# Optimization experiments

Measured on AMD Instinct MI355X. Metric: run time of the kernel, lower is better.

The kernel has to match this reference:

```python
import jax, jax.numpy as jnp
from jax import lax
import numpy as np

EPS = 1e-5

def _conv(x, w, b, s, p):
    # torch Conv2d: weight [O,I,kH,kW], NCHW
    y = lax.conv_general_dilated(x, w, (s, s), [(p, p), (p, p)],
                                 dimension_numbers=('NCHW', 'OIHW', 'NCHW'))
    return y + b[None, :, None, None]

def _convT(x, w, b, s, p):
    # torch ConvTranspose2d: weight [I,O,kH,kW]; equivalent to lhs-dilated conv
    wf = jnp.flip(w, (2, 3)).transpose(1, 0, 2, 3)  # -> [O,I,kH,kW]
    q = w.shape[2] - 1 - p
    y = lax.conv_general_dilated(x, wf, (1, 1), [(q, q), (q, q)],
                                 lhs_dilation=(s, s),
                                 dimension_numbers=('NCHW', 'OIHW', 'NCHW'))
    return y + b[None, :, None, None]

def _bn(x, g, b, m, v):
    # eval-mode BatchNorm2d with running stats
    s = g / jnp.sqrt(v + EPS)
    return x * s[None, :, None, None] + (b - m * s)[None, :, None, None]

def _forward(x, ew1, eb1, bn1g, bn1b, bn1m, bn1v, ew2, eb2, bn2g, bn2b, bn2m, bn2v,
             ew3, eb3, bn3g, bn3b, bn3m, bn3v, ew4, eb4, bn4g, bn4b, bn4m, bn4v,
             fc21w, fc21b, fc22w, fc22b, fc3w, fc3b,
             cw1, cb1, cbn1g, cbn1b, cbn1m, cbn1v, cw2, cb2, emb,
             dw1, db1, dbn1g, dbn1b, dbn1m, dbn1v, dw2, db2, dbn2g, dbn2b, dbn2m, dbn2v,
             dw3, db3, dbn3g, dbn3b, dbn3m, dbn3v, dw4, db4, dbn4g, dbn4b, dbn4m, dbn4v,
             ow, ob):
    relu = jax.nn.relu
    N = x.shape[0]
    # ---- encoder ----
    h = relu(_bn(_conv(x, ew1, eb1, 2, 1), bn1g, bn1b, bn1m, bn1v))   # [N,16,32,32]
    h = relu(_bn(_conv(h, ew2, eb2, 2, 1), bn2g, bn2b, bn2m, bn2v))   # [N,16,16,16]
    h = relu(_bn(_conv(h, ew3, eb3, 2, 1), bn3g, bn3b, bn3m, bn3v))   # [N,16,9,9]
    h = relu(_bn(_conv(h, ew4, eb4, 1, 0), bn4g, bn4b, bn4m, bn4v))   # [N,128,9,9]
    hl = h.reshape(N, -1)                                              # [N,10368]
    mu = hl @ fc21w + fc21b
    logvar = hl @ fc22w + fc22b
    z = mu  # eval-mode reparameterize returns mu
    # ---- vq_decode ----
    co = relu(z @ fc3w + fc3b)                                         # [N,10368]
    col = co.reshape(N, 128, 9, 9)
    ze = relu(_bn(_convT(col, cw1, cb1, 1, 0), cbn1g, cbn1b, cbn1m, cbn1v))
    z_e_x = _convT(ze, cw2, cb2, 1, 0)                                 # [N,32,9,9]
    zt = z_e_x.transpose(0, 2, 3, 1)                                   # [N,H,W,C]
    # ||z - e||^2 expanded (avoids [N,H,W,C,K] intermediate)
    d = ((zt * zt).sum(-1, keepdims=True)
         - 2.0 * jnp.einsum('nhwc,kc->nhwk', zt, emb)
         + (emb * emb).sum(-1))                                        # [N,H,W,K]
    latents = jnp.argmin(d, axis=-1)                                   # [N,H,W] int
    z_q = emb[latents]                                                 # [N,H,W,C]
    z_q_x = z_q.transpose(0, 3, 1, 2)                                  # [N,32,9,9]
    # ---- decoder ----
    g = relu(_bn(_convT(z_q_x, dw1, db1, 1, 0), dbn1g, dbn1b, dbn1m, dbn1v))  # [N,16,9,9]
    g = relu(_bn(_convT(g, dw2, db2, 2, 1), dbn2g, dbn2b, dbn2m, dbn2v))      # [N,16,18,18]
    g = relu(_bn(_convT(g, dw3, db3, 2, 1), dbn3g, dbn3b, dbn3m, dbn3v))      # [N,16,34,34]
    g = relu(_bn(_convT(g, dw4, db4, 2, 0), dbn4g, dbn4b, dbn4m, dbn4v))      # [N,16,68,68]
    x_tilde = _convT(g, ow, ob, 1, 0)                                         # [N,1,68,68]
    return (x_tilde, z, mu, logvar, z_e_x, z_q_x, latents)


def setup_inputs() -> dict:
    key = jax.random.key(0)
    ks = iter(jax.random.split(key, 64))
    def rn(shape, scale=0.05):
        return scale * jax.random.normal(next(ks), shape, jnp.float32)
    inp = {'x': jax.random.normal(next(ks), (512, 1, 64, 64), jnp.float32)}
    wspecs = {
        'ew1': (16, 1, 4, 4), 'eb1': (16,), 'ew2': (16, 16, 4, 4), 'eb2': (16,),
        'ew3': (16, 16, 2, 2), 'eb3': (16,), 'ew4': (128, 16, 1, 1), 'eb4': (128,),
        'fc21w': (10368, 64), 'fc21b': (64,), 'fc22w': (10368, 64), 'fc22b': (64,),
        'fc3w': (64, 10368), 'fc3b': (10368,),
        'cw1': (128, 32, 1, 1), 'cb1': (32,), 'cw2': (32, 32, 1, 1), 'cb2': (32,),
        'dw1': (32, 16, 1, 1), 'db1': (16,), 'dw2': (16, 16, 4, 4), 'db2': (16,),
        'dw3': (16, 16, 2, 2), 'db3': (16,), 'dw4': (16, 16, 2, 2), 'db4': (16,),
        'ow': (16, 1, 1, 1),
    }
    for n, s in wspecs.items():
        inp[n] = rn(s)
    inp['ob'] = jnp.full((1,), 0.5, jnp.float32)
    for ch, pre in [(16, 'bn1'), (16, 'bn2'), (16, 'bn3'), (128, 'bn4'), (32, 'cbn1'),
                    (16, 'dbn1'), (16, 'dbn2'), (16, 'dbn3'), (16, 'dbn4')]:
        inp[pre + 'g'] = jnp.ones((ch,), jnp.float32)
        inp[pre + 'b'] = jnp.zeros((ch,), jnp.float32)
        inp[pre + 'm'] = jnp.zeros((ch,), jnp.float32)
        inp[pre + 'v'] = jnp.ones((ch,), jnp.float32)
    inp['emb'] = rn((512, 32), 1.0 / 512)
    return inp


def reference(x, ew1, eb1, bn1g, bn1b, bn1m, bn1v, ew2, eb2, bn2g, bn2b, bn2m, bn2v,
              ew3, eb3, bn3g, bn3b, bn3m, bn3v, ew4, eb4, bn4g, bn4b, bn4m, bn4v,
              fc21w, fc21b, fc22w, fc22b, fc3w, fc3b,
              cw1, cb1, cbn1g, cbn1b, cbn1m, cbn1v, cw2, cb2, emb,
              dw1, db1, dbn1g, dbn1b, dbn1m, dbn1v, dw2, db2, dbn2g, dbn2b, dbn2m, dbn2v,
              dw3, db3, dbn3g, dbn3b, dbn3m, dbn3v, dw4, db4, dbn4g, dbn4b, dbn4m, dbn4v,
              ow, ob):
    return _forward(x, ew1, eb1, bn1g, bn1b, bn1m, bn1v, ew2, eb2, bn2g, bn2b, bn2m, bn2v,
                    ew3, eb3, bn3g, bn3b, bn3m, bn3v, ew4, eb4, bn4g, bn4b, bn4m, bn4v,
                    fc21w, fc21b, fc22w, fc22b, fc3w, fc3b,
                    cw1, cb1, cbn1g, cbn1b, cbn1m, cbn1v, cw2, cb2, emb,
                    dw1, db1, dbn1g, dbn1b, dbn1m, dbn1v, dw2, db2, dbn2g, dbn2b, dbn2m, dbn2v,
                    dw3, db3, dbn3g, dbn3b, dbn3m, dbn3v, dw4, db4, dbn4g, dbn4b, dbn4m, dbn4v,
                    ow, ob)
```

## Files before the change

kernel.cpp:

```cpp
#include <hip/hip_runtime.h>
#include <math.h>
#include <float.h>

#define BN_EPS 1e-5f

__device__ __forceinline__ float bn_apply(float y, float g, float b, float m, float v) {
  float s = g / sqrtf(v + BN_EPS);
  return y * s + (b - m * s);
}

__global__ void k_conv1(const float* __restrict__ x, const float* __restrict__ w,
                        const float* __restrict__ bias,
                        const float* __restrict__ g, const float* __restrict__ bb,
                        const float* __restrict__ bm, const float* __restrict__ bv,
                        float* __restrict__ out) {
  int t = blockIdx.x * 256 + threadIdx.x;
  int xo = t & 31, yo = (t >> 5) & 31, n = t >> 10;
  int iy0 = 2 * yo - 1, ix0 = 2 * xo - 1;
  const float* xb = x + n * 4096;
  float p[16];
#pragma unroll
  for (int ky = 0; ky < 4; ++ky)
#pragma unroll
    for (int kx = 0; kx < 4; ++kx) {
      int iy = iy0 + ky, ix = ix0 + kx;
      bool ok = (iy >= 0) & (iy < 64) & (ix >= 0) & (ix < 64);
      p[ky * 4 + kx] = ok ? xb[iy * 64 + ix] : 0.0f;
    }
  float* ob = out + n * 16384 + yo * 32 + xo;
#pragma unroll
  for (int o = 0; o < 16; ++o) {
    float acc = bias[o];
#pragma unroll
    for (int k = 0; k < 16; ++k) acc += p[k] * w[o * 16 + k];
    acc = bn_apply(acc, g[o], bb[o], bm[o], bv[o]);
    ob[o * 1024] = fmaxf(acc, 0.0f);
  }
}

__global__ void __launch_bounds__(256) k_conv2(const float* __restrict__ A,
                        const float* __restrict__ w, const float* __restrict__ bias,
                        const float* __restrict__ g, const float* __restrict__ bb,
                        const float* __restrict__ bm, const float* __restrict__ bv,
                        float* __restrict__ out) {
  int t = threadIdx.x;
  int lane = t & 63;
  int og = __builtin_amdgcn_readfirstlane(t >> 6);
  int idx = blockIdx.x * 64 + lane;
  int n = idx >> 8, p = idx & 255;
  int yo = p >> 4, xo = p & 15;
  int iy0 = 2 * yo - 1, ix0 = 2 * xo - 1;
  const float* Ab = A + n * 16384;
  float acc[4];
#pragma unroll
  for (int oo = 0; oo < 4; ++oo) acc[oo] = bias[og * 4 + oo];
  for (int i = 0; i < 16; ++i) {
    const float* ch = Ab + i * 1024;
    float pv[16];
#pragma unroll
    for (int ky = 0; ky < 4; ++ky)
#pragma unroll
      for (int kx = 0; kx < 4; ++kx) {
        int iy = iy0 + ky, ix = ix0 + kx;
        bool ok = (iy >= 0) & (iy < 32) & (ix >= 0) & (ix < 32);
        pv[ky * 4 + kx] = ok ? ch[iy * 32 + ix] : 0.0f;
      }
    const float* wb = w + ((og * 4) * 16 + i) * 16;
#pragma unroll
    for (int oo = 0; oo < 4; ++oo) {
      const float* wo = wb + oo * 256;
#pragma unroll
      for (int k = 0; k < 16; ++k) acc[oo] = fmaf(pv[k], wo[k], acc[oo]);
    }
  }
  float* ob = out + n * 4096 + p;
#pragma unroll
  for (int oo = 0; oo < 4; ++oo) {
    int o = og * 4 + oo;
    float s = g[o] / sqrtf(bv[o] + BN_EPS);
    float sh = bb[o] - bm[o] * s;
    ob[o * 256] = fmaxf(acc[oo] * s + sh, 0.0f);
  }
}

__global__ void __launch_bounds__(256) k_c34(const float* __restrict__ in,
    const float* __restrict__ w3, const float* __restrict__ b3,
    const float* __restrict__ g3, const float* __restrict__ bb3,
    const float* __restrict__ bm3, const float* __restrict__ bv3,
    const float* __restrict__ w4, const float* __restrict__ b4,
    const float* __restrict__ g4, const float* __restrict__ bb4,
    const float* __restrict__ bm4, const float* __restrict__ bv4,
    float* __restrict__ hl) {
  __shared__ float xin[4096];
  __shared__ float w3s[1024];
  __shared__ float c3s[16 * 81];
  __shared__ float k3a[16], k3b[16];
  __shared__ float k4a[128], k4b[128];
  int bx = blockIdx.x;
  int n = bx >> 1, half = bx & 1;
  int t = threadIdx.x;
  {
    const float4* iv = (const float4*)(in + n * 4096);
    float4* xv = (float4*)xin;
#pragma unroll
    for (int q = 0; q < 4; ++q) xv[t + 256 * q] = iv[t + 256 * q];
    for (int i = t; i < 1024; i += 256) w3s[i] = w3[i];
  }
  if (t < 16) {
    float s = g3[t] / sqrtf(bv3[t] + BN_EPS);
    k3a[t] = s;
    k3b[t] = b3[t] * s + (bb3[t] - bm3[t] * s);
  } else if (t >= 64 && t < 192) {
    int o = t - 64;
    float s = g4[o] / sqrtf(bv4[o] + BN_EPS);
    k4a[o] = s;
    k4b[o] = b4[o] * s + (bb4[o] - bm4[o] * s);
  }
  __syncthreads();
  for (int idx = t; idx < 1296; idx += 256) {
    int o = idx / 81, p = idx - o * 81;
    int yo = p / 9, xo = p - yo * 9;
    int iy0 = 2 * yo - 1, ix0 = 2 * xo - 1;
    bool ytop = iy0 >= 0, ybot = iy0 + 1 < 16;
    bool xlft = ix0 >= 0, xrgt = ix0 + 1 < 16;
    int iyt = ytop ? iy0 : 0, iyb = ybot ? iy0 + 1 : 15;
    int ixl = xlft ? ix0 : 0, ixr = xrgt ? ix0 + 1 : 15;
    float acc = 0.0f;
#pragma unroll
    for (int i = 0; i < 16; ++i) {
      const float* ch = xin + i * 256;
      float p0 = (ytop & xlft) ? ch[iyt * 16 + ixl] : 0.0f;
      float p1 = (ytop & xrgt) ? ch[iyt * 16 + ixr] : 0.0f;
      float p2 = (ybot & xlft) ? ch[iyb * 16 + ixl] : 0.0f;
      float p3 = (ybot & xrgt) ? ch[iyb * 16 + ixr] : 0.0f;
      float4 wv = *(const float4*)&w3s[(o * 16 + i) * 4];
      acc += p0 * wv.x + p1 * wv.y + p2 * wv.z + p3 * wv.w;
    }
    c3s[idx] = fmaxf(acc * k3a[o] + k3b[o], 0.0f);
  }
  __syncthreads();
  int lane = t & 63;
  int og = __builtin_amdgcn_readfirstlane(t >> 6);
  int o0 = half * 64 + og * 16;
  float* ob = hl + n * 10368;
#pragma unroll
  for (int pass = 0; pass < 2; ++pass) {
    int p = pass * 64 + lane;
    bool ok = p < 81; int pc = ok ? p : 80;
    float acc[16];
#pragma unroll
    for (int oo = 0; oo < 16; ++oo) acc[oo] = 0.0f;
#pragma unroll
    for (int i = 0; i < 16; ++i) {
      float v = c3s[i * 81 + pc];
#pragma unroll
      for (int oo = 0; oo < 16; ++oo)
        acc[oo] = fmaf(v, w4[(o0 + oo) * 16 + i], acc[oo]);
    }
    if (ok) {
#pragma unroll
      for (int oo = 0; oo < 16; ++oo) {
        int o = o0 + oo;
        ob[o * 81 + p] = fmaxf(acc[oo] * k4a[o] + k4b[o], 0.0f);
      }
    }
  }
}

__global__ void __launch_bounds__(256) k_gemm1(const float* __restrict__ hl,
                                               const float* __restrict__ w21,
                                               const float* __restrict__ w22,
                                               float* __restrict__ part) {
  __shared__ __align__(16) float hs[27 * 68];
  __shared__ __align__(16) float wsh[27 * 128];
  int kc = blockIdx.x, nt = blockIdx.y, t = threadIdx.x;
  int n0 = nt * 64, k0 = kc * 162;
  int jg = t & 31, ng = t >> 5;
  float acc[8][4];
#pragma unroll
  for (int i = 0; i < 8; ++i)
#pragma unroll
    for (int q = 0; q < 4; ++q) acc[i][q] = 0.0f;
  float ph[7], pw[14];
  {
    int ks = k0;
#pragma unroll
    for (int q = 0; q < 7; ++q) {
      int idx = t + q * 256;
      if (idx < 1728) { int nr = idx / 27, kk = idx - nr * 27;
        ph[q] = hl[(n0 + nr) * 10368 + ks + kk]; }
    }
#pragma unroll
    for (int q = 0; q < 14; ++q) {
      int idx = t + q * 256;
      if (idx < 3456) { int r = idx >> 7, c = idx & 127;
        pw[q] = (c < 64) ? w21[(ks + r) * 64 + c] : w22[(ks + r) * 64 + (c - 64)]; }
    }
  }
  for (int s = 0; s < 6; ++s) {
    __syncthreads();
#pragma unroll
    for (int q = 0; q < 7; ++q) {
      int idx = t + q * 256;
      if (idx < 1728) { int nr = idx / 27, kk = idx - nr * 27; hs[kk * 68 + nr] = ph[q]; }
    }
#pragma unroll
    for (int q = 0; q < 14; ++q) {
      int idx = t + q * 256;
      if (idx < 3456) wsh[idx] = pw[q];
    }
    __syncthreads();
    if (s < 5) {
      int ks = k0 + (s + 1) * 27;
#pragma unroll
      for (int q = 0; q < 7; ++q) {
        int idx = t + q * 256;
        if (idx < 1728) { int nr = idx / 27, kk = idx - nr * 27;
          ph[q] = hl[(n0 + nr) * 10368 + ks + kk]; }
      }
#pragma unroll
      for (int q = 0; q < 14; ++q) {
        int idx = t + q * 256;
        if (idx < 3456) { int r = idx >> 7, c = idx & 127;
          pw[q] = (c < 64) ? w21[(ks + r) * 64 + c] : w22[(ks + r) * 64 + (c - 64)]; }
      }
    }
#pragma unroll 9
    for (int kk = 0; kk < 27; ++kk) {
      float4 h0 = *(const float4*)&hs[kk * 68 + ng * 8];
      float4 h1 = *(const float4*)&hs[kk * 68 + ng * 8 + 4];
      float4 wv = *(const float4*)&wsh[kk * 128 + jg * 4];
      float hv[8] = {h0.x, h0.y, h0.z, h0.w, h1.x, h1.y, h1.z, h1.w};
#pragma unroll
      for (int i = 0; i < 8; ++i) {
        acc[i][0] = fmaf(hv[i], wv.x, acc[i][0]);
        acc[i][1] = fmaf(hv[i], wv.y, acc[i][1]);
        acc[i][2] = fmaf(hv[i], wv.z, acc[i][2]);
        acc[i][3] = fmaf(hv[i], wv.w, acc[i][3]);
      }
    }
  }
#pragma unroll
  for (int i = 0; i < 8; ++i) {
    int n = n0 + ng * 8 + i;
    *(float4*)&part[(size_t)(kc * 512 + n) * 128 + jg * 4] =
        make_float4(acc[i][0], acc[i][1], acc[i][2], acc[i][3]);
  }
}

__global__ void k_fc_red(const float* __restrict__ part, const float* __restrict__ b21,
                         const float* __restrict__ b22, float* __restrict__ z,
                         float* __restrict__ mu, float* __restrict__ lv) {
  int t = blockIdx.x * 256 + threadIdx.x;
  int j = t & 127, n = t >> 7;
  float s = 0.0f;
  for (int kc = 0; kc < 64; ++kc) s += part[(size_t)(kc * 512 + n) * 128 + j];
  if (j < 64) { float r = s + b21[j]; z[n * 64 + j] = r; mu[n * 64 + j] = r; }
  else        { lv[n * 64 + (j - 64)] = s + b22[j - 64]; }
}

__global__ void k_fc3(const float* __restrict__ z, const float* __restrict__ w,
                      const float* __restrict__ b, float* __restrict__ E) {
  int m = blockIdx.x * 128 + threadIdx.x;
  int n0 = blockIdx.y * 32;
  float acc[32];
#pragma unroll
  for (int nn = 0; nn < 32; ++nn) acc[nn] = 0.0f;
  for (int j = 0; j < 64; ++j) {
    float wv = w[j * 10368 + m];
    const float* zb = z + n0 * 64 + j;
#pragma unroll
    for (int nn = 0; nn < 32; ++nn) acc[nn] += zb[nn * 64] * wv;
  }
  float bvv = b[m];
  float* Eb = E + n0 * 10368 + m;
#pragma unroll
  for (int nn = 0; nn < 32; ++nn) Eb[nn * 10368] = fmaxf(acc[nn] + bvv, 0.0f);
}

__global__ void __launch_bounds__(256) k_cw(const float* __restrict__ E,
                     const float* __restrict__ w1, const float* __restrict__ b1,
                     const float* __restrict__ g, const float* __restrict__ bb,
                     const float* __restrict__ bm, const float* __restrict__ bv,
                     const float* __restrict__ w2, const float* __restrict__ b2,
                     float* __restrict__ zex, float* __restrict__ zt) {
  __shared__ float ze_s[2592];
  int n = blockIdx.x, t = threadIdx.x;
  int lane = t & 63;
  int o0 = __builtin_amdgcn_readfirstlane(t >> 6) * 8;
  const float* co = E + n * 10368;
#pragma unroll
  for (int pass = 0; pass < 2; ++pass) {
    int p = pass * 64 + lane;
    bool ok = p < 81; int pc = ok ? p : 80;
    float acc[8];
#pragma unroll
    for (int oo = 0; oo < 8; ++oo) acc[oo] = b1[o0 + oo];
    for (int i = 0; i < 128; ++i) {
      float v = co[i * 81 + pc];
#pragma unroll
      for (int oo = 0; oo < 8; ++oo)
        acc[oo] = fmaf(v, w1[i * 32 + o0 + oo], acc[oo]);
    }
#pragma unroll
    for (int oo = 0; oo < 8; ++oo) {
      int o = o0 + oo;
      float r = bn_apply(acc[oo], g[o], bb[o], bm[o], bv[o]);
      if (ok) ze_s[o * 81 + p] = fmaxf(r, 0.0f);
    }
  }
  __syncthreads();
  float* zb = zex + n * 2592;
  float* ztb = zt + n * 81 * 32;
#pragma unroll
  for (int pass = 0; pass < 2; ++pass) {
    int p = pass * 64 + lane;
    bool ok = p < 81; int pc = ok ? p : 80;
    float acc[8];
#pragma unroll
    for (int oo = 0; oo < 8; ++oo) acc[oo] = b2[o0 + oo];
    for (int j = 0; j < 32; ++j) {
      float v = ze_s[j * 81 + pc];
#pragma unroll
      for (int oo = 0; oo < 8; ++oo)
        acc[oo] = fmaf(v, w2[j * 32 + o0 + oo], acc[oo]);
    }
    if (ok) {
#pragma unroll
      for (int oo = 0; oo < 8; ++oo) {
        zb[(o0 + oo) * 81 + p] = acc[oo];
        ztb[p * 32 + o0 + oo] = acc[oo];
      }
    }
  }
}

__global__ void k_ee(const float* __restrict__ emb, float* __restrict__ ee) {
  int k = blockIdx.x * 256 + threadIdx.x;
  if (k < 512) {
    const float4* e = (const float4*)(emb + k * 32);
    float s = 0.0f;
#pragma unroll
    for (int q = 0; q < 8; ++q) {
      float4 v = e[q];
      s += v.x * v.x + v.y * v.y + v.z * v.z + v.w * v.w;
    }
    ee[k] = s;
  }
}

__global__ void __launch_bounds__(256) k_vq2(const float* __restrict__ zt,
                                             const float* __restrict__ emb,
                                             const float* __restrict__ ee,
                                             float* __restrict__ lat_out,
                                             float* __restrict__ zqx) {
  __shared__ float bd_s[4][64];
  __shared__ int   bi_s[4][64];
  __shared__ int   bif[64];
  int t = threadIdx.x;
  int lane = t & 63, sub = t >> 6;
  int sub_u = __builtin_amdgcn_readfirstlane(sub);
  int pix = blockIdx.x * 64 + lane;
  float z[32];
  {
    const float4* zr = (const float4*)(zt + (size_t)pix * 32);
#pragma unroll
    for (int q = 0; q < 8; ++q) {
      float4 v = zr[q];
      z[q * 4] = v.x; z[q * 4 + 1] = v.y; z[q * 4 + 2] = v.z; z[q * 4 + 3] = v.w;
    }
  }
  const float* ebase = emb + sub_u * 128 * 32;
  const float* eeb   = ee + sub_u * 128;
  int kbase = sub_u * 128;
  float best = FLT_MAX;
  int bi = kbase;
  for (int kk = 0; kk < 128; kk += 2) {
    const float* e0 = ebase + kk * 32;
    const float* e1 = e0 + 32;
    float d0a = 0.f, d0b = 0.f, d1a = 0.f, d1b = 0.f;
#pragma unroll
    for (int c = 0; c < 32; c += 2) {
      d0a = fmaf(z[c], e0[c], d0a);
      d0b = fmaf(z[c + 1], e0[c + 1], d0b);
      d1a = fmaf(z[c], e1[c], d1a);
      d1b = fmaf(z[c + 1], e1[c + 1], d1b);
    }
    float d0 = fmaf(-2.0f, d0a + d0b, eeb[kk]);
    float d1 = fmaf(-2.0f, d1a + d1b, eeb[kk + 1]);
    if (d0 < best) { best = d0; bi = kbase + kk; }
    if (d1 < best) { best = d1; bi = kbase + kk + 1; }
  }
  bd_s[sub][lane] = best;
  bi_s[sub][lane] = bi;
  __syncthreads();
  if (t < 64) {
    float bd = bd_s[0][t]; int b = bi_s[0][t];
#pragma unroll
    for (int q = 1; q < 4; ++q)
      if (bd_s[q][t] < bd) { bd = bd_s[q][t]; b = bi_s[q][t]; }
    lat_out[blockIdx.x * 64 + t] = (float)b;
    bif[t] = b;
  }
  __syncthreads();
  int pix0 = blockIdx.x * 64;
  for (int idx = t; idx < 2048; idx += 256) {
    int c = idx >> 6, pl = idx & 63;
    int pg = pix0 + pl;
    int n = pg / 81, p = pg - n * 81;
    zqx[n * 2592 + c * 81 + p] = emb[bif[pl] * 32 + c];
  }
}

__global__ void k_dw1(const float* __restrict__ in, const float* __restrict__ w,
                      const float* __restrict__ bias,
                      const float* __restrict__ g, const float* __restrict__ bb,
                      const float* __restrict__ bm, const float* __restrict__ bv,
                      float* __restrict__ out) {
  __shared__ float ws[512];
  for (int i = threadIdx.x; i < 512; i += 256) ws[i] = w[i];
  __syncthreads();
  int t = blockIdx.x * 256 + threadIdx.x;
  int p = t % 81; int o = (t / 81) & 15; int n = t / 1296;
  const float* ib = in + n * 2592 + p;
  float acc = bias[o];
#pragma unroll
  for (int i = 0; i < 32; ++i) acc += ib[i * 81] * ws[i * 16 + o];
  float r = bn_apply(acc, g[o], bb[o], bm[o], bv[o]);
  out[t] = fmaxf(r, 0.0f);
}

__global__ void __launch_bounds__(256) k_dw2(const float* __restrict__ in,
                      const float* __restrict__ w, const float* __restrict__ bias,
                      const float* __restrict__ g, const float* __restrict__ bb,
                      const float* __restrict__ bm, const float* __restrict__ bv,
                      float* __restrict__ out) {
  int t = threadIdx.x;
  int lane = t & 63;
  int og = __builtin_amdgcn_readfirstlane(t >> 6);
  int idx = blockIdx.x * 64 + lane;
  int n = idx / 81, blk = idx - n * 81;
  int iy = blk / 9, ix = blk - iy * 9;
  const float* ib = in + n * 1296;
  int r0 = iy - 1, r2 = iy + 1, c0 = ix - 1, c2 = ix + 1;
  bool r0ok = r0 >= 0, r2ok = r2 < 9, c0ok = c0 >= 0, c2ok = c2 < 9;
  int r0c = r0ok ? r0 : 0, r2c = r2ok ? r2 : 8;
  int c0c = c0ok ? c0 : 0, c2c = c2ok ? c2 : 8;
  float acc[4][2][2];
#pragma unroll
  for (int oo = 0; oo < 4; ++oo)
#pragma unroll
    for (int dy = 0; dy < 2; ++dy)
#pragma unroll
      for (int dx = 0; dx < 2; ++dx) acc[oo][dy][dx] = 0.0f;
  for (int i = 0; i < 16; ++i) {
    const float* ch = ib + i * 81;
    float v[3][3];
    v[1][1] = ch[iy * 9 + ix];
    v[1][0] = c0ok ? ch[iy * 9 + c0c] : 0.0f;
    v[1][2] = c2ok ? ch[iy * 9 + c2c] : 0.0f;
    v[0][1] = r0ok ? ch[r0c * 9 + ix] : 0.0f;
    v[0][0] = (r0ok & c0ok) ? ch[r0c * 9 + c0c] : 0.0f;
    v[0][2] = (r0ok & c2ok) ? ch[r0c * 9 + c2c] : 0.0f;
    v[2][1] = r2ok ? ch[r2c * 9 + ix] : 0.0f;
    v[2][0] = (r2ok & c0ok) ? ch[r2c * 9 + c0c] : 0.0f;
    v[2][2] = (r2ok & c2ok) ? ch[r2c * 9 + c2c] : 0.0f;
    const float* wb = w + (i * 16 + og * 4) * 16;
#pragma unroll
    for (int oo = 0; oo < 4; ++oo) {
      const float* wo = wb + oo * 16;
      acc[oo][0][0] = fmaf(v[1][1], wo[1 * 4 + 1], acc[oo][0][0]);
      acc[oo][0][0] = fmaf(v[1][0], wo[1 * 4 + 3], acc[oo][0][0]);
      acc[oo][0][0] = fmaf(v[0][1], wo[3 * 4 + 1], acc[oo][0][0]);
      acc[oo][0][0] = fmaf(v[0][0], wo[3 * 4 + 3], acc[oo][0][0]);
      acc[oo][0][1] = fmaf(v[1][1], wo[1 * 4 + 2], acc[oo][0][1]);
      acc[oo][0][1] = fmaf(v[1][2], wo[1 * 4 + 0], acc[oo][0][1]);
      acc[oo][0][1] = fmaf(v[0][1], wo[3 * 4 + 2], acc[oo][0][1]);
      acc[oo][0][1] = fmaf(v[0][2], wo[3 * 4 + 0], acc[oo][0][1]);
      acc[oo][1][0] = fmaf(v[1][1], wo[2 * 4 + 1], acc[oo][1][0]);
      acc[oo][1][0] = fmaf(v[1][0], wo[2 * 4 + 3], acc[oo][1][0]);
      acc[oo][1][0] = fmaf(v[2][1], wo[0 * 4 + 1], acc[oo][1][0]);
      acc[oo][1][0] = fmaf(v[2][0], wo[0 * 4 + 3], acc[oo][1][0]);
      acc[oo][1][1] = fmaf(v[1][1], wo[2 * 4 + 2], acc[oo][1][1]);
      acc[oo][1][1] = fmaf(v[1][2], wo[2 * 4 + 0], acc[oo][1][1]);
      acc[oo][1][1] = fmaf(v[2][1], wo[0 * 4 + 2], acc[oo][1][1]);
      acc[oo][1][1] = fmaf(v[2][2], wo[0 * 4 + 0], acc[oo][1][1]);
    }
  }
  float* ob = out + n * 5184 + (2 * iy) * 18 + 2 * ix;
#pragma unroll
  for (int oo = 0; oo < 4; ++oo) {
    int o = og * 4 + oo;
    float s = g[o] / sqrtf(bv[o] + BN_EPS);
    float sh = bb[o] - bm[o] * s;
    float bo = bias[o];
    float r00 = fmaxf((acc[oo][0][0] + bo) * s + sh, 0.0f);
    float r01 = fmaxf((acc[oo][0][1] + bo) * s + sh, 0.0f);
    float r10 = fmaxf((acc[oo][1][0] + bo) * s + sh, 0.0f);
    float r11 = fmaxf((acc[oo][1][1] + bo) * s + sh, 0.0f);
    float* op = ob + o * 324;
    *(float2*)&op[0]  = make_float2(r00, r01);
    *(float2*)&op[18] = make_float2(r10, r11);
  }
}

__global__ void k_dw3(const float* __restrict__ in, const float* __restrict__ w,
                      const float* __restrict__ bias,
                      const float* __restrict__ g, const float* __restrict__ bb,
                      const float* __restrict__ bm, const float* __restrict__ bv,
                      float* __restrict__ out) {
  int t = blockIdx.x * 256 + threadIdx.x;
  int ii = t % 324; int n = t / 324;
  int iy = ii / 18, ix = ii % 18;
  const float* ib = in + n * 5184 + iy * 18 + ix;
  float acc[4][16];
#pragma unroll
  for (int a = 0; a < 4; ++a)
#pragma unroll
    for (int o = 0; o < 16; ++o) acc[a][o] = 0.0f;
  for (int i = 0; i < 16; ++i) {
    float v = ib[i * 324];
    const float4* wr = (const float4*)(w + i * 64);
#pragma unroll
    for (int o = 0; o < 16; ++o) {
      float4 wt = wr[o];
      acc[0][o] = fmaf(v, wt.x, acc[0][o]);
      acc[1][o] = fmaf(v, wt.y, acc[1][o]);
      acc[2][o] = fmaf(v, wt.z, acc[2][o]);
      acc[3][o] = fmaf(v, wt.w, acc[3][o]);
    }
  }
  int yo0 = 2 * iy - 1, xo0 = 2 * ix - 1;
  float* ob = out + n * 18496;
#pragma unroll
  for (int o = 0; o < 16; ++o) {
    float s = g[o] / sqrtf(bv[o] + BN_EPS);
    float sh = bb[o] - bm[o] * s;
    float bo = bias[o];
#pragma unroll
    for (int a = 0; a < 2; ++a)
#pragma unroll
      for (int b = 0; b < 2; ++b) {
        int yo = yo0 + a, xo = xo0 + b;
        if (yo >= 0 && yo < 34 && xo >= 0 && xo < 34)
          ob[o * 1156 + yo * 34 + xo] = fmaxf((acc[a * 2 + b][o] + bo) * s + sh, 0.0f);
      }
  }
}

__global__ void k_dw4ow(const float* __restrict__ in, const float* __restrict__ w,
                        const float* __restrict__ bias,
                        const float* __restrict__ g, const float* __restrict__ bb,
                        const float* __restrict__ bm, const float* __restrict__ bv,
                        const float* __restrict__ oww, const float* __restrict__ obb,
                        float* __restrict__ out) {
  int t = blockIdx.x * 256 + threadIdx.x;
  int ii = t % 1156; int n = t / 1156;
  int iy = ii / 34, ix = ii % 34;
  const float* ib = in + n * 18496 + iy * 34 + ix;
  float acc[4][16];
#pragma unroll
  for (int a = 0; a < 4; ++a)
#pragma unroll
    for (int o = 0; o < 16; ++o) acc[a][o] = 0.0f;
  for (int i = 0; i < 16; ++i) {
    float v = ib[i * 1156];
    const float4* wr = (const float4*)(w + i * 64);
#pragma unroll
    for (int o = 0; o < 16; ++o) {
      float4 wt = wr[o];
      acc[0][o] = fmaf(v, wt.x, acc[0][o]);
      acc[1][o] = fmaf(v, wt.y, acc[1][o]);
      acc[2][o] = fmaf(v, wt.z, acc[2][o]);
      acc[3][o] = fmaf(v, wt.w, acc[3][o]);
    }
  }
  float r[4];
#pragma unroll
  for (int a = 0; a < 4; ++a) r[a] = obb[0];
#pragma unroll
  for (int o = 0; o < 16; ++o) {
    float s = g[o] / sqrtf(bv[o] + BN_EPS);
    float sh = bb[o] - bm[o] * s;
    float bo = bias[o];
    float wo = oww[o];
#pragma unroll
    for (int a = 0; a < 4; ++a)
      r[a] += fmaxf((acc[a][o] + bo) * s + sh, 0.0f) * wo;
  }
  float* ob = out + n * 4624 + 2 * ix;
  *(float2*)&ob[(2 * iy) * 68]     = make_float2(r[0], r[1]);
  *(float2*)&ob[(2 * iy + 1) * 68] = make_float2(r[2], r[3]);
}

extern "C" void kernel_launch(void* const* d_in, const int* in_sizes, int n_in,
                              void* d_out, int out_size, void* d_ws, size_t ws_size,
                              hipStream_t stream) {
  const float* x     = (const float*)d_in[0];
  const float* ew1   = (const float*)d_in[1];
  const float* eb1   = (const float*)d_in[2];
  const float* ew2   = (const float*)d_in[3];
  const float* eb2   = (const float*)d_in[4];
  const float* ew3   = (const float*)d_in[5];
  const float* eb3   = (const float*)d_in[6];
  const float* ew4   = (const float*)d_in[7];
  const float* eb4   = (const float*)d_in[8];
  const float* fc21w = (const float*)d_in[9];
  const float* fc21b = (const float*)d_in[10];
  const float* fc22w = (const float*)d_in[11];
  const float* fc22b = (const float*)d_in[12];
  const float* fc3w  = (const float*)d_in[13];
  const float* fc3b  = (const float*)d_in[14];
  const float* cw1   = (const float*)d_in[15];
  const float* cb1   = (const float*)d_in[16];
  const float* cw2   = (const float*)d_in[17];
  const float* cb2   = (const float*)d_in[18];
  const float* dw1   = (const float*)d_in[19];
  const float* db1   = (const float*)d_in[20];
  const float* dw2   = (const float*)d_in[21];
  const float* db2   = (const float*)d_in[22];
  const float* dw3   = (const float*)d_in[23];
  const float* db3   = (const float*)d_in[24];
  const float* dw4   = (const float*)d_in[25];
  const float* db4   = (const float*)d_in[26];
  const float* oww   = (const float*)d_in[27];
  const float* obb   = (const float*)d_in[28];
  const float* bn1g  = (const float*)d_in[29];
  const float* bn1b  = (const float*)d_in[30];
  const float* bn1m  = (const float*)d_in[31];
  const float* bn1v  = (const float*)d_in[32];
  const float* bn2g  = (const float*)d_in[33];
  const float* bn2b  = (const float*)d_in[34];
  const float* bn2m  = (const float*)d_in[35];
  const float* bn2v  = (const float*)d_in[36];
  const float* bn3g  = (const float*)d_in[37];
  const float* bn3b  = (const float*)d_in[38];
  const float* bn3m  = (const float*)d_in[39];
  const float* bn3v  = (const float*)d_in[40];
  const float* bn4g  = (const float*)d_in[41];
  const float* bn4b  = (const float*)d_in[42];
  const float* bn4m  = (const float*)d_in[43];
  const float* bn4v  = (const float*)d_in[44];
  const float* cbn1g = (const float*)d_in[45];
  const float* cbn1b = (const float*)d_in[46];
  const float* cbn1m = (const float*)d_in[47];
  const float* cbn1v = (const float*)d_in[48];
  const float* dbn1g = (const float*)d_in[49];
  const float* dbn1b = (const float*)d_in[50];
  const float* dbn1m = (const float*)d_in[51];
  const float* dbn1v = (const float*)d_in[52];
  const float* dbn2g = (const float*)d_in[53];
  const float* dbn2b = (const float*)d_in[54];
  const float* dbn2m = (const float*)d_in[55];
  const float* dbn2v = (const float*)d_in[56];
  const float* dbn3g = (const float*)d_in[57];
  const float* dbn3b = (const float*)d_in[58];
  const float* dbn3m = (const float*)d_in[59];
  const float* dbn3v = (const float*)d_in[60];
  const float* dbn4g = (const float*)d_in[61];
  const float* dbn4b = (const float*)d_in[62];
  const float* dbn4m = (const float*)d_in[63];
  const float* dbn4v = (const float*)d_in[64];
  const float* emb   = (const float*)d_in[65];

  float* out = (float*)d_out;
  float* xt_o  = out;
  float* z_o   = out + 2367488;
  float* mu_o  = out + 2400256;
  float* lv_o  = out + 2433024;
  float* zex_o = out + 2465792;
  float* zqx_o = out + 3792896;
  float* lat_o = out + 5120000;

  float* ws = (float*)d_ws;
  float* A    = ws;
  float* Bt   = ws + 8388608;
  float* Dhl  = ws + 663552;
  float* part = ws + 5971968;
  float* Eco  = ws;
  float* zt   = ws + 10166272;
  float* eev  = ws + 11493376;
  float* G    = ws + 5308416;
  float* H    = ws + 5971968;
  float* I    = ws + 8626176;

  k_conv1<<<2048, 256, 0, stream>>>(x, ew1, eb1, bn1g, bn1b, bn1m, bn1v, A);
  k_conv2<<<2048, 256, 0, stream>>>(A, ew2, eb2, bn2g, bn2b, bn2m, bn2v, Bt);
  k_c34<<<1024, 256, 0, stream>>>(Bt, ew3, eb3, bn3g, bn3b, bn3m, bn3v,
                                  ew4, eb4, bn4g, bn4b, bn4m, bn4v, Dhl);
  k_gemm1<<<dim3(64, 8), 256, 0, stream>>>(Dhl, fc21w, fc22w, part);
  k_fc_red<<<256, 256, 0, stream>>>(part, fc21b, fc22b, z_o, mu_o, lv_o);
  k_ee<<<2, 256, 0, stream>>>(emb, eev);
  k_fc3<<<dim3(81, 16), 128, 0, stream>>>(z_o, fc3w, fc3b, Eco);
  k_cw<<<512, 256, 0, stream>>>(Eco, cw1, cb1, cbn1g, cbn1b, cbn1m, cbn1v, cw2, cb2, zex_o, zt);
  k_vq2<<<648, 256, 0, stream>>>(zt, emb, eev, lat_o, zqx_o);
  k_dw1<<<2592, 256, 0, stream>>>(zqx_o, dw1, db1, dbn1g, dbn1b, dbn1m, dbn1v, G);
  k_dw2<<<648, 256, 0, stream>>>(G, dw2, db2, dbn2g, dbn2b, dbn2m, dbn2v, H);
  k_dw3<<<648, 256, 0, stream>>>(H, dw3, db3, dbn3g, dbn3b, dbn3m, dbn3v, I);
  k_dw4ow<<<2312, 256, 0, stream>>>(I, dw4, db4, dbn4g, dbn4b, dbn4m, dbn4v, oww, obb, xt_o);
}
```

Before: 488.4 us.

## Store conv1 output as zero-padded NHWC to vectorize conv2 loads

conv1 now writes its activations in a channels-last layout with a one-pixel zero border, using float4 stores. A new kernel zeroes that border, and another reorders the conv2 weights so each tap is a contiguous block. conv2 then reads 16 channels per tap as four float4 loads with no bounds checks, instead of doing a predicated scalar gather per channel. This adds two small launches and reshuffles the workspace offsets. conv1's stores now stride 64 bytes per lane, so they are less coalesced.

```diff
diff --git a/kernel.cpp b/kernel.cpp
--- a/kernel.cpp
+++ b/kernel.cpp
@@ -7,13 +7,34 @@
 __device__ __forceinline__ float bn_apply(float y, float g, float b, float m, float v) {
   float s = g / sqrtf(v + BN_EPS);
   return y * s + (b - m * s);
+}
+
+__global__ void k_pad0(float* __restrict__ A) {
+  int n = blockIdx.x, t = threadIdx.x;
+  if (t >= 132) return;
+  int r, c;
+  if (t < 34)       { r = 0;        c = t; }
+  else if (t < 68)  { r = 33;       c = t - 34; }
+  else if (t < 100) { r = t - 67;   c = 0; }
+  else              { r = t - 99;   c = 33; }
+  float4* p = (float4*)(A + n * 18496 + (r * 34 + c) * 16);
+  float4 z = make_float4(0.f, 0.f, 0.f, 0.f);
+  p[0] = z; p[1] = z; p[2] = z; p[3] = z;
+}
+
+__global__ void k_wr2(const float* __restrict__ w, float* __restrict__ wr2) {
+  int idx = blockIdx.x * 256 + threadIdx.x;
+  int og = idx >> 10, rem = idx & 1023;
+  int tap = rem >> 6, r2 = rem & 63;
+  int i = r2 >> 2, oo = r2 & 3;
+  wr2[idx] = w[(og * 4 + oo) * 256 + i * 16 + tap];
 }
 
 __global__ void k_conv1(const float* __restrict__ x, const float* __restrict__ w,
                         const float* __restrict__ bias,
                         const float* __restrict__ g, const float* __restrict__ bb,
                         const float* __restrict__ bm, const float* __restrict__ bv,
-                        float* __restrict__ out) {
+                        float* __restrict__ A) {
   int t = blockIdx.x * 256 + threadIdx.x;
   int xo = t & 31, yo = (t >> 5) & 31, n = t >> 10;
   int iy0 = 2 * yo - 1, ix0 = 2 * xo - 1;
@@ -27,19 +48,24 @@
       bool ok = (iy >= 0) & (iy < 64) & (ix >= 0) & (ix < 64);
       p[ky * 4 + kx] = ok ? xb[iy * 64 + ix] : 0.0f;
     }
-  float* ob = out + n * 16384 + yo * 32 + xo;
+  float r[16];
 #pragma unroll
   for (int o = 0; o < 16; ++o) {
     float acc = bias[o];
 #pragma unroll
     for (int k = 0; k < 16; ++k) acc += p[k] * w[o * 16 + k];
     acc = bn_apply(acc, g[o], bb[o], bm[o], bv[o]);
-    ob[o * 1024] = fmaxf(acc, 0.0f);
-  }
+    r[o] = fmaxf(acc, 0.0f);
+  }
+  float* ob = A + n * 18496 + ((yo + 1) * 34 + (xo + 1)) * 16;
+  *(float4*)&ob[0]  = make_float4(r[0], r[1], r[2], r[3]);
+  *(float4*)&ob[4]  = make_float4(r[4], r[5], r[6], r[7]);
+  *(float4*)&ob[8]  = make_float4(r[8], r[9], r[10], r[11]);
+  *(float4*)&ob[12] = make_float4(r[12], r[13], r[14], r[15]);
 }
 
 __global__ void __launch_bounds__(256) k_conv2(const float* __restrict__ A,
-                        const float* __restrict__ w, const float* __restrict__ bias,
+                        const float* __restrict__ wr2, const float* __restrict__ bias,
                         const float* __restrict__ g, const float* __restrict__ bb,
                         const float* __restrict__ bm, const float* __restrict__ bv,
                         float* __restrict__ out) {
@@ -49,30 +75,27 @@
   int idx = blockIdx.x * 64 + lane;
   int n = idx >> 8, p = idx & 255;
   int yo = p >> 4, xo = p & 15;
-  int iy0 = 2 * yo - 1, ix0 = 2 * xo - 1;
-  const float* Ab = A + n * 16384;
+  const float* Ab = A + n * 18496 + (2 * yo * 34 + 2 * xo) * 16;
+  const float* wb = wr2 + og * 1024;
   float acc[4];
 #pragma unroll
   for (int oo = 0; oo < 4; ++oo) acc[oo] = bias[og * 4 + oo];
-  for (int i = 0; i < 16; ++i) {
-    const float* ch = Ab + i * 1024;
-    float pv[16];
-#pragma unroll
-    for (int ky = 0; ky < 4; ++ky)
-#pragma unroll
-      for (int kx = 0; kx < 4; ++kx) {
-        int iy = iy0 + ky, ix = ix0 + kx;
-        bool ok = (iy >= 0) & (iy < 32) & (ix >= 0) & (ix < 32);
-        pv[ky * 4 + kx] = ok ? ch[iy * 32 + ix] : 0.0f;
+#pragma unroll
+  for (int ky = 0; ky < 4; ++ky)
+#pragma unroll
+    for (int kx = 0; kx < 4; ++kx) {
+      const float4* tp = (const float4*)(Ab + (ky * 34 + kx) * 16);
+      float4 a0 = tp[0], a1 = tp[1], a2 = tp[2], a3 = tp[3];
+      const float* wt = wb + (ky * 4 + kx) * 64;
+      float pv[16] = {a0.x, a0.y, a0.z, a0.w, a1.x, a1.y, a1.z, a1.w,
+                      a2.x, a2.y, a2.z, a2.w, a3.x, a3.y, a3.z, a3.w};
+#pragma unroll
+      for (int i = 0; i < 16; ++i) {
+#pragma unroll
+        for (int oo = 0; oo < 4; ++oo)
+          acc[oo] = fmaf(pv[i], wt[i * 4 + oo], acc[oo]);
       }
-    const float* wb = w + ((og * 4) * 16 + i) * 16;
-#pragma unroll
-    for (int oo = 0; oo < 4; ++oo) {
-      const float* wo = wb + oo * 256;
-#pragma unroll
-      for (int k = 0; k < 16; ++k) acc[oo] = fmaf(pv[k], wo[k], acc[oo]);
-    }
-  }
+    }
   float* ob = out + n * 4096 + p;
 #pragma unroll
   for (int oo = 0; oo < 4; ++oo) {
@@ -674,18 +697,21 @@
 
   float* ws = (float*)d_ws;
   float* A    = ws;
-  float* Bt   = ws + 8388608;
-  float* Dhl  = ws + 663552;
-  float* part = ws + 5971968;
+  float* Bt   = ws + 9469952;
+  float* Dhl  = ws;
+  float* part = ws + 9469952;
   float* Eco  = ws;
-  float* zt   = ws + 10166272;
-  float* eev  = ws + 11493376;
-  float* G    = ws + 5308416;
-  float* H    = ws + 5971968;
-  float* I    = ws + 8626176;
-
+  float* zt   = ws + 9469952;
+  float* G    = ws + 9469952;
+  float* H    = ws + 10133504;
+  float* I    = ws;
+  float* eev  = ws + 13664256;
+  float* wr2  = ws + 13664768;
+
+  k_pad0<<<512, 256, 0, stream>>>(A);
+  k_wr2<<<16, 256, 0, stream>>>(ew2, wr2);
   k_conv1<<<2048, 256, 0, stream>>>(x, ew1, eb1, bn1g, bn1b, bn1m, bn1v, A);
-  k_conv2<<<2048, 256, 0, stream>>>(A, ew2, eb2, bn2g, bn2b, bn2m, bn2v, Bt);
+  k_conv2<<<2048, 256, 0, stream>>>(A, wr2, eb2, bn2g, bn2b, bn2m, bn2v, Bt);
   k_c34<<<1024, 256, 0, stream>>>(Bt, ew3, eb3, bn3g, bn3b, bn3m, bn3v,
                                   ew4, eb4, bn4g, bn4b, bn4m, bn4v, Dhl);
   k_gemm1<<<dim3(64, 8), 256, 0, stream>>>(Dhl, fc21w, fc22w, part);
```

After: 501.8 us. 2.8% more time.
